# Optimization experiments

Measured on AMD Instinct MI355X. Metric: run time of the kernel, lower is better.

Reference implementation:

```python
import jax, jax.numpy as jnp
import numpy as np

V, C, T_BLK, H, L = 65, 512, 256, 8, 8
HS = C // H
EPS = 1e-5


def _ln(x, g, b):
    m = jnp.mean(x, axis=-1, keepdims=True)
    v = jnp.mean((x - m) ** 2, axis=-1, keepdims=True)
    return (x - m) * jax.lax.rsqrt(v + EPS) * g + b


def setup_inputs() -> dict:
    key = jax.random.key(0)
    ks = jax.random.split(key, 16)
    B, T = 64, 256
    idx = jax.random.randint(ks[0], (B, T), 0, V)
    targets = jax.random.randint(ks[1], (B, T), 0, V)
    n = lambda k, shape, s: (jax.random.normal(k, shape, dtype=jnp.float32) * s)
    return {
        "idx": idx,
        "targets": targets,
        "tok_emb": n(ks[2], (V, C), 0.02),
        "pos_emb": n(ks[3], (T_BLK, C), 0.02),
        "ln1_g": jnp.ones((L, C), jnp.float32),
        "ln1_b": jnp.zeros((L, C), jnp.float32),
        "wq": n(ks[4], (L, C, C), (2.0 / C) ** 0.5),
        "wk": n(ks[5], (L, C, C), (2.0 / C) ** 0.5),
        "wv": n(ks[6], (L, C, C), (2.0 / C) ** 0.5),
        "wo": n(ks[7], (L, C, C), (2.0 / C) ** 0.5),
        "bo": jnp.zeros((L, C), jnp.float32),
        "ln2_g": jnp.ones((L, C), jnp.float32),
        "ln2_b": jnp.zeros((L, C), jnp.float32),
        "w1": n(ks[8], (L, C, 4 * C), (2.0 / C) ** 0.5),
        "b1": jnp.zeros((L, 4 * C), jnp.float32),
        "w2": n(ks[9], (L, 4 * C, C), (2.0 / (4 * C)) ** 0.5),
        "b2": jnp.zeros((L, C), jnp.float32),
        "lnf_g": jnp.ones((C,), jnp.float32),
        "lnf_b": jnp.zeros((C,), jnp.float32),
        "lm_w": n(ks[10], (C, V), (2.0 / C) ** 0.5),
        "lm_b": jnp.zeros((V,), jnp.float32),
    }


def _gpt_forward(tok_emb, pos_emb, ln1_g, ln1_b, wq, wk, wv, wo, bo,
                 ln2_g, ln2_b, w1, b1, w2, b2, lnf_g, lnf_b, lm_w, lm_b,
                 idx, targets):
    B, T = idx.shape
    x = tok_emb[idx] + pos_emb[:T]  # [B,T,C]
    causal = jnp.tril(jnp.ones((T, T), bool))
    scale = float(C) ** -0.5  # NOTE: scaled by n_embd, not head_size (faithful)
    for l in range(L):
        h = _ln(x, ln1_g[l], ln1_b[l])
        q = (h @ wq[l]).reshape(B, T, H, HS)
        k = (h @ wk[l]).reshape(B, T, H, HS)
        v = (h @ wv[l]).reshape(B, T, H, HS)
        scores = jnp.einsum('bthd,bshd->bhts', q, k) * scale
        scores = jnp.where(causal, scores, -jnp.inf)
        w = jax.nn.softmax(scores, axis=-1)
        attn = jnp.einsum('bhts,bshd->bthd', w, v).reshape(B, T, C)
        x = x + attn @ wo[l] + bo[l]
        h2 = _ln(x, ln2_g[l], ln2_b[l])
        x = x + jax.nn.relu(h2 @ w1[l] + b1[l]) @ w2[l] + b2[l]
    x = _ln(x, lnf_g, lnf_b)
    logits = (x @ lm_w + lm_b).reshape(B * T, V)
    logp = jax.nn.log_softmax(logits, axis=-1)
    tgt = targets.reshape(B * T)
    loss = -jnp.mean(jnp.take_along_axis(logp, tgt[:, None], axis=-1))
    return logits, loss


def reference(idx, targets, tok_emb, pos_emb, ln1_g, ln1_b, wq, wk, wv, wo, bo,
              ln2_g, ln2_b, w1, b1, w2, b2, lnf_g, lnf_b, lm_w, lm_b):
    return _gpt_forward(tok_emb, pos_emb, ln1_g, ln1_b, wq, wk, wv, wo, bo,
                        ln2_g, ln2_b, w1, b1, w2, b2, lnf_g, lnf_b, lm_w, lm_b,
                        idx, targets)
```

## Files before the change

### kernel.cpp

```cpp
#include <hip/hip_runtime.h>
#include <math.h>

#define V_SZ   65
#define C_DIM  512
#define T_SEQ  256
#define H_N    8
#define HS_D   64
#define L_N    8
#define N_TOK  16384
#define LN_EPS 1e-5f
#define SM_SCALE 0.044194173824159216f

typedef unsigned short ushortT;
typedef __attribute__((ext_vector_type(8))) short    short8;
typedef __attribute__((ext_vector_type(8))) ushortT  ushort8;
typedef __attribute__((ext_vector_type(4))) float    f32x4;

typedef __attribute__((address_space(3))) unsigned int        lds_uint;
typedef const __attribute__((address_space(1))) unsigned int  glob_uint;

__device__ inline ushortT f2bf(float f) {
    unsigned int u = __float_as_uint(f);
    u = (u + 0x7fffu + ((u >> 16) & 1u)) >> 16;
    return (ushortT)u;
}
__device__ inline float bf2f(ushortT u) {
    return __uint_as_float(((unsigned int)u) << 16);
}

__global__ void embed_kernel(const int* __restrict__ idx,
                             const float* __restrict__ tok,
                             const float* __restrict__ pos,
                             float* __restrict__ x) {
    int i = blockIdx.x * blockDim.x + threadIdx.x;
    const int NF4 = N_TOK * C_DIM / 4;
    if (i >= NF4) return;
    int c4 = i % (C_DIM / 4);
    int n  = i / (C_DIM / 4);
    int t  = n % T_SEQ;
    int tk = idx[n];
    float4 a = ((const float4*)tok)[(size_t)tk * (C_DIM/4) + c4];
    float4 p = ((const float4*)pos)[(size_t)t  * (C_DIM/4) + c4];
    float4 r; r.x=a.x+p.x; r.y=a.y+p.y; r.z=a.z+p.z; r.w=a.w+p.w;
    ((float4*)x)[i] = r;
}

__global__ __launch_bounds__(256) void tcast_kernel(const float* __restrict__ src,
                                                    ushortT* __restrict__ dst,
                                                    int K, int N) {
    __shared__ float tile[32][33];
    size_t lo = (size_t)blockIdx.z * K * N;
    int n0 = blockIdx.x * 32, k0 = blockIdx.y * 32;
    int tx = threadIdx.x & 31, ty = threadIdx.x >> 5;
    #pragma unroll
    for (int s = 0; s < 4; s++) {
        int kk = ty + s * 8;
        tile[kk][tx] = src[lo + (size_t)(k0 + kk) * N + n0 + tx];
    }
    __syncthreads();
    #pragma unroll
    for (int s = 0; s < 4; s++) {
        int nn = ty + s * 8;
        dst[lo + (size_t)(n0 + nn) * K + k0 + tx] = f2bf(tile[tx][nn]);
    }
}

__global__ __launch_bounds__(256) void lmcast_kernel(const float* __restrict__ w,
                                                     ushortT* __restrict__ dst) {
    int n = blockIdx.x;
    for (int k = threadIdx.x; k < C_DIM; k += 256)
        dst[(size_t)n * C_DIM + k] = (n < V_SZ) ? f2bf(w[(size_t)k * V_SZ + n]) : (ushortT)0;
}

template<bool BF16OUT>
__global__ __launch_bounds__(256) void ln_kernel(const float* __restrict__ in,
                                                 const float* __restrict__ g,
                                                 const float* __restrict__ b,
                                                 void* __restrict__ outv) {
    int wave = threadIdx.x >> 6;
    int lane = threadIdx.x & 63;
    int row  = blockIdx.x * 4 + wave;
    const float4* r4 = (const float4*)(in + (size_t)row * C_DIM);
    float v[8];
    *(float4*)&v[0] = r4[lane * 2];
    *(float4*)&v[4] = r4[lane * 2 + 1];
    float s = 0.f;
    #pragma unroll
    for (int k = 0; k < 8; k++) s += v[k];
    #pragma unroll
    for (int m = 32; m >= 1; m >>= 1) s += __shfl_xor(s, m, 64);
    float mean = s * (1.0f / C_DIM);
    float vs = 0.f;
    #pragma unroll
    for (int k = 0; k < 8; k++) { float d = v[k] - mean; vs += d * d; }
    #pragma unroll
    for (int m = 32; m >= 1; m >>= 1) vs += __shfl_xor(vs, m, 64);
    float rstd = rsqrtf(vs * (1.0f / C_DIM) + LN_EPS);
    float gv[8], bv[8];
    *(float4*)&gv[0] = *(const float4*)&g[lane * 8];
    *(float4*)&gv[4] = *(const float4*)&g[lane * 8 + 4];
    *(float4*)&bv[0] = *(const float4*)&b[lane * 8];
    *(float4*)&bv[4] = *(const float4*)&b[lane * 8 + 4];
    if (BF16OUT) {
        ushort8 pack;
        #pragma unroll
        for (int k = 0; k < 8; k++) pack[k] = f2bf((v[k] - mean) * rstd * gv[k] + bv[k]);
        *(ushort8*)&((ushortT*)outv)[(size_t)row * C_DIM + lane * 8] = pack;
    } else {
        float o[8];
        #pragma unroll
        for (int k = 0; k < 8; k++) o[k] = (v[k] - mean) * rstd * gv[k] + bv[k];
        float4* o4 = (float4*)&((float*)outv)[(size_t)row * C_DIM + lane * 8];
        o4[0] = *(float4*)&o[0];
        o4[1] = *(float4*)&o[4];
    }
}

template<int EPI>
__device__ __forceinline__ void gemm_core(const ushortT* __restrict__ A,
                                          const ushortT* __restrict__ Bt,
                                          const float* __restrict__ bias,
                                          const float* __restrict__ res,
                                          void* __restrict__ outp,
                                          int N, int K,
                                          int mBase, int nBase) {
    __shared__ __align__(16) ushortT As[128 * 32];
    __shared__ __align__(16) ushortT Bs[128 * 32];
    const int tid = threadIdx.x;
    const int w = tid >> 6, lane = tid & 63;
    const int wr = w >> 1, wc = w & 1;
    const int l15 = lane & 15, lg = lane >> 4;

    const int srow = (lane >> 2);
    const int sslot = lane & 3;

    f32x4 acc[4][4];
    #pragma unroll
    for (int i = 0; i < 4; i++)
        #pragma unroll
        for (int j = 0; j < 4; j++)
            acc[i][j] = {0.f, 0.f, 0.f, 0.f};

    for (int k0 = 0; k0 < K; k0 += 32) {
        #pragma unroll
        for (int t = 0; t < 2; t++) {
            int r = w * 32 + t * 16 + srow;
            int ks = sslot ^ ((r >> 1) & 3);
            const ushortT* ga = &A[(size_t)(mBase + r) * K + k0 + ks * 8];
            __builtin_amdgcn_global_load_lds((glob_uint*)ga,
                (lds_uint*)&As[(w * 32 + t * 16) * 32], 16, 0, 0);
            const ushortT* gb = &Bt[(size_t)(nBase + r) * K + k0 + ks * 8];
            __builtin_amdgcn_global_load_lds((glob_uint*)gb,
                (lds_uint*)&Bs[(w * 32 + t * 16) * 32], 16, 0, 0);
        }
        __syncthreads();
        short8 af[4], bfr[4];
        #pragma unroll
        for (int i = 0; i < 4; i++) {
            int r = wr * 64 + i * 16 + l15;
            int cb = (lg * 16) ^ (((r >> 1) & 3) << 4);
            af[i] = *(const short8*)((const char*)As + r * 64 + cb);
        }
        #pragma unroll
        for (int j = 0; j < 4; j++) {
            int r = wc * 64 + j * 16 + l15;
            int cb = (lg * 16) ^ (((r >> 1) & 3) << 4);
            bfr[j] = *(const short8*)((const char*)Bs + r * 64 + cb);
        }
        #pragma unroll
        for (int i = 0; i < 4; i++)
            #pragma unroll
            for (int j = 0; j < 4; j++)
                acc[i][j] = __builtin_amdgcn_mfma_f32_16x16x32_bf16(af[i], bfr[j], acc[i][j], 0, 0, 0);
        __syncthreads();
    }

    int lr = lg * 4;
    #pragma unroll
    for (int i = 0; i < 4; i++) {
        #pragma unroll
        for (int j = 0; j < 4; j++) {
            int col = nBase + wc * 64 + j * 16 + l15;
            if (EPI == 4 && col >= V_SZ) continue;
            #pragma unroll
            for (int q = 0; q < 4; q++) {
                size_t row = (size_t)(mBase + wr * 64 + i * 16 + lr + q);
                float vv = acc[i][j][q];
                if (EPI >= 2) vv += bias[col];
                if (EPI == 2) vv = fmaxf(vv, 0.f);
                if (EPI == 3) vv += res[row * N + col];
                if (EPI == 1)      ((ushortT*)outp)[row * N + col] = f2bf(vv);
                else if (EPI == 2) ((ushortT*)outp)[row * N + col] = f2bf(vv);
                else if (EPI == 3) ((float*)outp)[row * N + col]   = vv;
                else               ((float*)outp)[row * V_SZ + col] = vv;
            }
        }
    }
}

template<int EPI>
__global__ __launch_bounds__(256, 2) void gemm_bf16(const ushortT* __restrict__ A,
                                                    const ushortT* __restrict__ Bt,
                                                    const float* __restrict__ bias,
                                                    const float* __restrict__ res,
                                                    void* __restrict__ outp,
                                                    int N, int K) {
    gemm_core<EPI>(A, Bt, bias, res, outp, N, K, blockIdx.x * 128, blockIdx.y * 128);
}

__global__ __launch_bounds__(256, 2) void gemm_qkv(const ushortT* __restrict__ A,
                                                   const ushortT* __restrict__ bq,
                                                   const ushortT* __restrict__ bk,
                                                   const ushortT* __restrict__ bv,
                                                   ushortT* __restrict__ oq,
                                                   ushortT* __restrict__ ok,
                                                   ushortT* __restrict__ ov,
                                                   int N, int K) {
    const ushortT* Bt = (blockIdx.z == 0) ? bq : (blockIdx.z == 1) ? bk : bv;
    ushortT*       o  = (blockIdx.z == 0) ? oq : (blockIdx.z == 1) ? ok : ov;
    gemm_core<1>(A, Bt, nullptr, nullptr, o, N, K, blockIdx.x * 128, blockIdx.y * 128);
}

__global__ __launch_bounds__(256) void attn_kernel(const ushortT* __restrict__ qp,
                                                   const ushortT* __restrict__ kp,
                                                   const ushortT* __restrict__ vp,
                                                   ushortT* __restrict__ att) {
    __shared__ ushortT K_lds[T_SEQ][72];
    __shared__ ushortT Vt_lds[HS_D][264];
    __shared__ ushortT P_lds[4][16][72];
    int bh = blockIdx.x;
    int b = bh >> 3, h = bh & 7;
    int tid = threadIdx.x;
    int w = tid >> 6, lane = tid & 63;
    const size_t rowbase = (size_t)b * T_SEQ * C_DIM + (size_t)h * HS_D;
    int l15 = lane & 15, lg = lane >> 4;

    #pragma unroll
    for (int it = 0; it < 8; it++) {
        int f = tid + it * 256;
        int r = f >> 3, c8 = f & 7;
        ushort8 kb = *(const ushort8*)&kp[rowbase + (size_t)r * C_DIM + c8 * 8];
        *(ushort8*)&K_lds[r][c8 * 8] = kb;
        ushort8 vb = *(const ushort8*)&vp[rowbase + (size_t)r * C_DIM + c8 * 8];
        #pragma unroll
        for (int e = 0; e < 8; e++) Vt_lds[c8 * 8 + e][r] = vb[e];
    }

    short8 qf[4][2];
    #pragma unroll
    for (int i = 0; i < 4; i++) {
        int grow = 16 * (4 * i + w) + l15;
        #pragma unroll
        for (int kk = 0; kk < 2; kk++)
            qf[i][kk] = *(const short8*)&qp[rowbase + (size_t)grow * C_DIM + kk * 32 + lg * 8];
    }
    __syncthreads();

    f32x4 acc_o[4][4];
    float mrun[4][4], lrun[4][4];
    #pragma unroll
    for (int i = 0; i < 4; i++) {
        #pragma unroll
        for (int j = 0; j < 4; j++) acc_o[i][j] = {0.f, 0.f, 0.f, 0.f};
        #pragma unroll
        for (int q = 0; q < 4; q++) { mrun[i][q] = -1e30f; lrun[i][q] = 0.f; }
    }

    #pragma unroll
    for (int jt = 0; jt < 4; jt++) {
        #pragma unroll
        for (int i = 0; i < 4; i++) {
            if (i < jt) continue;
            f32x4 acc_s[4];
            #pragma unroll
            for (int j_ = 0; j_ < 4; j_++) acc_s[j_] = {0.f, 0.f, 0.f, 0.f};
            #pragma unroll
            for (int j_ = 0; j_ < 4; j_++)
                #pragma unroll
                for (int kk = 0; kk < 2; kk++) {
                    short8 kf = *(const short8*)&K_lds[jt * 64 + j_ * 16 + l15][kk * 32 + lg * 8];
                    acc_s[j_] = __builtin_amdgcn_mfma_f32_16x16x32_bf16(qf[i][kk], kf, acc_s[j_], 0, 0, 0);
                }
            float sv[4][4];
            #pragma unroll
            for (int j_ = 0; j_ < 4; j_++) {
                int colg = jt * 64 + j_ * 16 + l15;
                #pragma unroll
                for (int q = 0; q < 4; q++) {
                    int rowg = 16 * (4 * i + w) + lg * 4 + q;
                    float s = acc_s[j_][q] * SM_SCALE;
                    sv[j_][q] = (i == jt && colg > rowg) ? -1e30f : s;
                }
            }
            #pragma unroll
            for (int q = 0; q < 4; q++) {
                float mx = fmaxf(fmaxf(sv[0][q], sv[1][q]), fmaxf(sv[2][q], sv[3][q]));
                #pragma unroll
                for (int msk = 1; msk <= 8; msk <<= 1) mx = fmaxf(mx, __shfl_xor(mx, msk, 64));
                float mold = mrun[i][q];
                float mnew = fmaxf(mold, mx);
                float corr = __expf(mold - mnew);
                mrun[i][q] = mnew;
                float ps = 0.f;
                #pragma unroll
                for (int j_ = 0; j_ < 4; j_++) {
                    float pe = __expf(sv[j_][q] - mnew);
                    ps += pe;
                    P_lds[w][lg * 4 + q][j_ * 16 + l15] = f2bf(pe);
                }
                lrun[i][q] = lrun[i][q] * corr + ps;
                #pragma unroll
                for (int dj = 0; dj < 4; dj++) acc_o[i][dj][q] *= corr;
            }
            short8 pa[2];
            #pragma unroll
            for (int kk = 0; kk < 2; kk++)
                pa[kk] = *(const short8*)&P_lds[w][l15][kk * 32 + lg * 8];
            #pragma unroll
            for (int dj = 0; dj < 4; dj++)
                #pragma unroll
                for (int kk = 0; kk < 2; kk++) {
                    short8 vf = *(const short8*)&Vt_lds[dj * 16 + l15][jt * 64 + kk * 32 + lg * 8];
                    acc_o[i][dj] = __builtin_amdgcn_mfma_f32_16x16x32_bf16(pa[kk], vf, acc_o[i][dj], 0, 0, 0);
                }
        }
    }

    #pragma unroll
    for (int i = 0; i < 4; i++) {
        float inv[4];
        #pragma unroll
        for (int q = 0; q < 4; q++) {
            float ls = lrun[i][q];
            #pragma unroll
            for (int msk = 1; msk <= 8; msk <<= 1) ls += __shfl_xor(ls, msk, 64);
            inv[q] = 1.0f / ls;
        }
        #pragma unroll
        for (int dj = 0; dj < 4; dj++) {
            int colg = dj * 16 + l15;
            #pragma unroll
            for (int q = 0; q < 4; q++) {
                int rowg = 16 * (4 * i + w) + lg * 4 + q;
                att[rowbase + (size_t)rowg * C_DIM + colg] = f2bf(acc_o[i][dj][q] * inv[q]);
            }
        }
    }
}

__global__ __launch_bounds__(256) void rowloss_kernel(const float* __restrict__ logits,
                                                      const int* __restrict__ tgt,
                                                      float* __restrict__ rl) {
    int wave = threadIdx.x >> 6, lane = threadIdx.x & 63;
    int n = blockIdx.x * 4 + wave;
    const float* l = logits + (size_t)n * V_SZ;
    float v0 = l[lane];
    float v1 = (lane == 0) ? l[64] : -1e30f;
    float m = fmaxf(v0, v1);
    #pragma unroll
    for (int s = 32; s >= 1; s >>= 1) m = fmaxf(m, __shfl_xor(m, s, 64));
    float e = __expf(v0 - m) + ((lane == 0) ? __expf(v1 - m) : 0.f);
    #pragma unroll
    for (int s = 32; s >= 1; s >>= 1) e += __shfl_xor(e, s, 64);
    if (lane == 0) {
        float lp = l[tgt[n]] - m - logf(e);
        rl[n] = -lp;
    }
}

__global__ __launch_bounds__(256) void reduce_loss_kernel(const float* __restrict__ rl,
                                                          float* __restrict__ out_loss) {
    __shared__ float sdata[256];
    float s = 0.f;
    for (int i = threadIdx.x; i < N_TOK; i += 256) s += rl[i];
    sdata[threadIdx.x] = s;
    __syncthreads();
    for (int st = 128; st > 0; st >>= 1) {
        if (threadIdx.x < st) sdata[threadIdx.x] += sdata[threadIdx.x + st];
        __syncthreads();
    }
    if (threadIdx.x == 0) out_loss[0] = sdata[0] * (1.0f / N_TOK);
}

extern "C" void kernel_launch(void* const* d_in, const int* in_sizes, int n_in,
                              void* d_out, int out_size, void* d_ws, size_t ws_size,
                              hipStream_t stream) {
    const int*   idx     = (const int*)d_in[0];
    const int*   targets = (const int*)d_in[1];
    const float* tok_emb = (const float*)d_in[2];
    const float* pos_emb = (const float*)d_in[3];
    const float* ln1_g   = (const float*)d_in[4];
    const float* ln1_b   = (const float*)d_in[5];
    const float* wq      = (const float*)d_in[6];
    const float* wk      = (const float*)d_in[7];
    const float* wv      = (const float*)d_in[8];
    const float* wo      = (const float*)d_in[9];
    const float* bo      = (const float*)d_in[10];
    const float* ln2_g   = (const float*)d_in[11];
    const float* ln2_b   = (const float*)d_in[12];
    const float* w1      = (const float*)d_in[13];
    const float* b1      = (const float*)d_in[14];
    const float* w2      = (const float*)d_in[15];
    const float* b2      = (const float*)d_in[16];
    const float* lnf_g   = (const float*)d_in[17];
    const float* lnf_b   = (const float*)d_in[18];
    const float* lm_w    = (const float*)d_in[19];
    const float* lm_b    = (const float*)d_in[20];

    float* out = (float*)d_out;
    char*  ws  = (char*)d_ws;
    const size_t MB = 1024ull * 1024ull;
    float*   x     = (float*)(ws);
    ushortT* h_bf  = (ushortT*)(ws + 32 * MB);
    ushortT* q_bf  = (ushortT*)(ws + 48 * MB);
    ushortT* k_bf  = (ushortT*)(ws + 64 * MB);
    ushortT* v_bf  = (ushortT*)(ws + 80 * MB);
    ushortT* att_bf= (ushortT*)(ws + 112 * MB);
    ushortT* ff1_bf= (ushortT*)(ws + 48 * MB);
    ushortT* wqT   = (ushortT*)(ws + 128 * MB);
    ushortT* wkT   = (ushortT*)(ws + 132 * MB);
    ushortT* wvT   = (ushortT*)(ws + 136 * MB);
    ushortT* woT   = (ushortT*)(ws + 140 * MB);
    ushortT* w1T   = (ushortT*)(ws + 144 * MB);
    ushortT* w2T   = (ushortT*)(ws + 160 * MB);
    float*   rl    = (float*)(ws + 176 * MB);
    ushortT* lmT   = (ushortT*)(ws + 177 * MB);

    {
        dim3 gCC(C_DIM / 32, C_DIM / 32, L_N);
        tcast_kernel<<<gCC, 256, 0, stream>>>(wq, wqT, C_DIM, C_DIM);
        tcast_kernel<<<gCC, 256, 0, stream>>>(wk, wkT, C_DIM, C_DIM);
        tcast_kernel<<<gCC, 256, 0, stream>>>(wv, wvT, C_DIM, C_DIM);
        tcast_kernel<<<gCC, 256, 0, stream>>>(wo, woT, C_DIM, C_DIM);
        dim3 g1(4 * C_DIM / 32, C_DIM / 32, L_N);
        tcast_kernel<<<g1, 256, 0, stream>>>(w1, w1T, C_DIM, 4 * C_DIM);
        dim3 g2(C_DIM / 32, 4 * C_DIM / 32, L_N);
        tcast_kernel<<<g2, 256, 0, stream>>>(w2, w2T, 4 * C_DIM, C_DIM);
        lmcast_kernel<<<128, 256, 0, stream>>>(lm_w, lmT);
    }

    embed_kernel<<<(N_TOK * C_DIM / 4 + 255) / 256, 256, 0, stream>>>(idx, tok_emb, pos_emb, x);

    dim3 gemmCC(N_TOK / 128, C_DIM / 128);
    dim3 gemmC4(N_TOK / 128, 4 * C_DIM / 128);
    dim3 gemmQKV(N_TOK / 128, C_DIM / 128, 3);

    for (int l = 0; l < L_N; l++) {
        const ushortT* wqT_l = wqT + (size_t)l * C_DIM * C_DIM;
        const ushortT* wkT_l = wkT + (size_t)l * C_DIM * C_DIM;
        const ushortT* wvT_l = wvT + (size_t)l * C_DIM * C_DIM;
        const ushortT* woT_l = woT + (size_t)l * C_DIM * C_DIM;
        const ushortT* w1T_l = w1T + (size_t)l * C_DIM * 4 * C_DIM;
        const ushortT* w2T_l = w2T + (size_t)l * C_DIM * 4 * C_DIM;

        ln_kernel<true><<<N_TOK / 4, 256, 0, stream>>>(x, ln1_g + l * C_DIM, ln1_b + l * C_DIM, h_bf);
        gemm_qkv<<<gemmQKV, 256, 0, stream>>>(h_bf, wqT_l, wkT_l, wvT_l, q_bf, k_bf, v_bf, C_DIM, C_DIM);
        attn_kernel<<<64 * H_N, 256, 0, stream>>>(q_bf, k_bf, v_bf, att_bf);
        gemm_bf16<3><<<gemmCC, 256, 0, stream>>>(att_bf, woT_l, bo + l * C_DIM, x, x, C_DIM, C_DIM);
        ln_kernel<true><<<N_TOK / 4, 256, 0, stream>>>(x, ln2_g + l * C_DIM, ln2_b + l * C_DIM, h_bf);
        gemm_bf16<2><<<gemmC4, 256, 0, stream>>>(h_bf, w1T_l, b1 + (size_t)l * 4 * C_DIM, nullptr, ff1_bf, 4 * C_DIM, C_DIM);
        gemm_bf16<3><<<gemmCC, 256, 0, stream>>>(ff1_bf, w2T_l, b2 + l * C_DIM, x, x, C_DIM, 4 * C_DIM);
    }

    ln_kernel<true><<<N_TOK / 4, 256, 0, stream>>>(x, lnf_g, lnf_b, h_bf);
    gemm_bf16<4><<<dim3(N_TOK / 128, 1), 256, 0, stream>>>(h_bf, lmT, lm_b, nullptr, out, V_SZ, C_DIM);

    rowloss_kernel<<<N_TOK / 4, 256, 0, stream>>>(out, targets, rl);
    reduce_loss_kernel<<<1, 256, 0, stream>>>(rl, out + (size_t)N_TOK * V_SZ);
}
```

Before: 1.728 ms.

## Add double-buffered K=64 GEMM kernel for output and FFN2 projections

Introduces a new GEMM kernel that stages 64-wide K tiles into double-buffered LDS with an XOR swizzle. The next tile's global-to-LDS loads are issued while the current tile's MFMAs run. It is used for the attention output projection and the second FFN GEMM, both of which have N=512 and only 512 blocks. LDS use grows to 64KB per block, which may reduce occupancy, and the epilogue still writes scalar, uncoalesced stores.

```diff
diff --git a/kernel.cpp b/kernel.cpp
--- a/kernel.cpp
+++ b/kernel.cpp
@@ -130,7 +130,6 @@
     const int w = tid >> 6, lane = tid & 63;
     const int wr = w >> 1, wc = w & 1;
     const int l15 = lane & 15, lg = lane >> 4;
-
     const int srow = (lane >> 2);
     const int sslot = lane & 3;
 
@@ -219,6 +218,108 @@
     const ushortT* Bt = (blockIdx.z == 0) ? bq : (blockIdx.z == 1) ? bk : bv;
     ushortT*       o  = (blockIdx.z == 0) ? oq : (blockIdx.z == 1) ? ok : ov;
     gemm_core<1>(A, Bt, nullptr, nullptr, o, N, K, blockIdx.x * 128, blockIdx.y * 128);
+}
+
+template<int EPI>
+__global__ __launch_bounds__(256, 2) void gemm_k64(const ushortT* __restrict__ A,
+                                                   const ushortT* __restrict__ Bt,
+                                                   const float* __restrict__ bias,
+                                                   const float* __restrict__ res,
+                                                   void* __restrict__ outp,
+                                                   int N, int K) {
+    __shared__ __align__(16) ushortT As[2][128 * 64];
+    __shared__ __align__(16) ushortT Bs[2][128 * 64];
+    const int tid = threadIdx.x;
+    const int w = tid >> 6, lane = tid & 63;
+    const int wr = w >> 1, wc = w & 1;
+    const int l15 = lane & 15, lg = lane >> 4;
+    const int mBase = blockIdx.x * 128, nBase = blockIdx.y * 128;
+    const int NT = K >> 6;
+    const int srow = lane >> 3;
+    const int sgran = lane & 7;
+
+    f32x4 acc[4][4];
+    #pragma unroll
+    for (int i = 0; i < 4; i++)
+        #pragma unroll
+        for (int j = 0; j < 4; j++)
+            acc[i][j] = {0.f, 0.f, 0.f, 0.f};
+
+    auto stage = [&](int buf, int k0) {
+        #pragma unroll
+        for (int t = 0; t < 4; t++) {
+            int r = w * 32 + t * 8 + srow;
+            int gl = sgran ^ (r & 7);
+            const ushortT* ga = &A[(size_t)(mBase + r) * K + k0 + gl * 8];
+            __builtin_amdgcn_global_load_lds((glob_uint*)ga,
+                (lds_uint*)&As[buf][(w * 32 + t * 8) * 64], 16, 0, 0);
+            const ushortT* gb = &Bt[(size_t)(nBase + r) * K + k0 + gl * 8];
+            __builtin_amdgcn_global_load_lds((glob_uint*)gb,
+                (lds_uint*)&Bs[buf][(w * 32 + t * 8) * 64], 16, 0, 0);
+        }
+    };
+
+    stage(0, 0);
+    int cur = 0;
+    for (int t = 0; t < NT; t++) {
+        asm volatile("s_waitcnt vmcnt(0)" ::: "memory");
+        __builtin_amdgcn_s_barrier();
+        __builtin_amdgcn_sched_barrier(0);
+        if (t + 1 < NT) stage(cur ^ 1, (t + 1) * 64);
+
+        const char* as = (const char*)&As[cur][0];
+        const char* bs = (const char*)&Bs[cur][0];
+        short8 af[2][4], bfr[2][4];
+        #pragma unroll
+        for (int i = 0; i < 4; i++) {
+            int r = wr * 64 + i * 16 + l15;
+            #pragma unroll
+            for (int kk = 0; kk < 2; kk++) {
+                int g = (kk * 4 + lg) ^ (r & 7);
+                af[kk][i] = *(const short8*)(as + r * 128 + g * 16);
+            }
+        }
+        #pragma unroll
+        for (int j = 0; j < 4; j++) {
+            int r = wc * 64 + j * 16 + l15;
+            #pragma unroll
+            for (int kk = 0; kk < 2; kk++) {
+                int g = (kk * 4 + lg) ^ (r & 7);
+                bfr[kk][j] = *(const short8*)(bs + r * 128 + g * 16);
+            }
+        }
+        __builtin_amdgcn_s_setprio(1);
+        #pragma unroll
+        for (int kk = 0; kk < 2; kk++)
+            #pragma unroll
+            for (int i = 0; i < 4; i++)
+                #pragma unroll
+                for (int j = 0; j < 4; j++)
+                    acc[i][j] = __builtin_amdgcn_mfma_f32_16x16x32_bf16(af[kk][i], bfr[kk][j], acc[i][j], 0, 0, 0);
+        __builtin_amdgcn_s_setprio(0);
+        asm volatile("s_waitcnt lgkmcnt(0)" ::: "memory");
+        cur ^= 1;
+    }
+
+    int lr = lg * 4;
+    #pragma unroll
+    for (int i = 0; i < 4; i++) {
+        #pragma unroll
+        for (int j = 0; j < 4; j++) {
+            int col = nBase + wc * 64 + j * 16 + l15;
+            #pragma unroll
+            for (int q = 0; q < 4; q++) {
+                size_t row = (size_t)(mBase + wr * 64 + i * 16 + lr + q);
+                float vv = acc[i][j][q];
+                if (EPI >= 2) vv += bias[col];
+                if (EPI == 2) vv = fmaxf(vv, 0.f);
+                if (EPI == 3) vv += res[row * N + col];
+                if (EPI == 1)      ((ushortT*)outp)[row * N + col] = f2bf(vv);
+                else if (EPI == 2) ((ushortT*)outp)[row * N + col] = f2bf(vv);
+                else               ((float*)outp)[row * N + col]   = vv;
+            }
+        }
+    }
 }
 
 __global__ __launch_bounds__(256) void attn_kernel(const ushortT* __restrict__ qp,
@@ -456,10 +557,10 @@
         ln_kernel<true><<<N_TOK / 4, 256, 0, stream>>>(x, ln1_g + l * C_DIM, ln1_b + l * C_DIM, h_bf);
         gemm_qkv<<<gemmQKV, 256, 0, stream>>>(h_bf, wqT_l, wkT_l, wvT_l, q_bf, k_bf, v_bf, C_DIM, C_DIM);
         attn_kernel<<<64 * H_N, 256, 0, stream>>>(q_bf, k_bf, v_bf, att_bf);
-        gemm_bf16<3><<<gemmCC, 256, 0, stream>>>(att_bf, woT_l, bo + l * C_DIM, x, x, C_DIM, C_DIM);
+        gemm_k64<3><<<gemmCC, 256, 0, stream>>>(att_bf, woT_l, bo + l * C_DIM, x, x, C_DIM, C_DIM);
         ln_kernel<true><<<N_TOK / 4, 256, 0, stream>>>(x, ln2_g + l * C_DIM, ln2_b + l * C_DIM, h_bf);
         gemm_bf16<2><<<gemmC4, 256, 0, stream>>>(h_bf, w1T_l, b1 + (size_t)l * 4 * C_DIM, nullptr, ff1_bf, 4 * C_DIM, C_DIM);
-        gemm_bf16<3><<<gemmCC, 256, 0, stream>>>(ff1_bf, w2T_l, b2 + l * C_DIM, x, x, C_DIM, 4 * C_DIM);
+        gemm_k64<3><<<gemmCC, 256, 0, stream>>>(ff1_bf, w2T_l, b2 + l * C_DIM, x, x, C_DIM, 4 * C_DIM);
     }
 
     ln_kernel<true><<<N_TOK / 4, 256, 0, stream>>>(x, lnf_g, lnf_b, h_bf);
```

After: 1.670 ms. -3.3%, faster.
